# Optimization experiments

Hardware: AMD Instinct MI355X
Metric: run time of the kernel (lower is better)

Reference implementation:

```python
import jax, jax.numpy as jnp
import numpy as np

B, T, D = 2, 2048, 2048
HQ, HKV, HD = 16, 8, 128
GROUP = HQ // HKV
EPS = 1e-6


def rms_norm(x, scale):
    # qwen3-compatible: compute in fp32
    xf = x.astype(jnp.float32)
    var = jnp.mean(xf * xf, axis=-1, keepdims=True)
    return (xf * jax.lax.rsqrt(var + EPS) * scale).astype(x.dtype)


def apply_rope(x, cos, sin):
    # x: [B,H,T,d]; cos,sin: [T,d]
    d2 = x.shape[-1] // 2
    x1, x2 = x[..., :d2], x[..., d2:]
    rot = jnp.concatenate([-x2, x1], axis=-1)
    return (x * cos[None, None] + rot * sin[None, None]).astype(x.dtype)


def setup_inputs() -> dict:
    key = jax.random.key(0)
    ks = jax.random.split(key, 8)
    x = jax.random.normal(ks[0], (B, T, D), dtype=jnp.float32)
    # causal mask: True where attention is disallowed (j > i)
    mask = jnp.triu(jnp.ones((T, T), dtype=jnp.bool_), k=1)
    # RoPE tables
    inv_freq = 1.0 / (10000.0 ** (np.arange(0, HD, 2, dtype=np.float32) / HD))
    pos = np.arange(T, dtype=np.float32)
    ang = np.outer(pos, inv_freq)  # [T, HD/2]
    ang = np.concatenate([ang, ang], axis=-1)  # [T, HD]
    cos = jnp.asarray(np.cos(ang), dtype=jnp.float32)
    sin = jnp.asarray(np.sin(ang), dtype=jnp.float32)
    s = 0.02
    Wq = jax.random.normal(ks[1], (HQ * HD, D), dtype=jnp.float32) * s
    Wk = jax.random.normal(ks[2], (HKV * HD, D), dtype=jnp.float32) * s
    Wv = jax.random.normal(ks[3], (HKV * HD, D), dtype=jnp.float32) * s
    Wo = jax.random.normal(ks[4], (D, HQ * HD), dtype=jnp.float32) * s
    q_scale = jnp.ones((HD,), dtype=jnp.float32)
    k_scale = jnp.ones((HD,), dtype=jnp.float32)
    return {"x": x, "mask": mask, "cos": cos, "sin": sin,
            "Wq": Wq, "Wk": Wk, "Wv": Wv, "Wo": Wo,
            "q_scale": q_scale, "k_scale": k_scale}


def reference(x, mask, cos, sin, Wq, Wk, Wv, Wo, q_scale, k_scale):
    Bc, Tc, _ = x.shape
    Q = jnp.einsum('btd,ed->bte', x, Wq).reshape(Bc, Tc, HQ, HD).transpose(0, 2, 1, 3)
    K = jnp.einsum('btd,ed->bte', x, Wk).reshape(Bc, Tc, HKV, HD).transpose(0, 2, 1, 3)
    V = jnp.einsum('btd,ed->bte', x, Wv).reshape(Bc, Tc, HKV, HD).transpose(0, 2, 1, 3)
    Q = rms_norm(Q, q_scale)
    K = rms_norm(K, k_scale)
    Q = apply_rope(Q, cos, sin)
    K = apply_rope(K, cos, sin)
    K = jnp.repeat(K, GROUP, axis=1)  # [B,HQ,T,d]
    V = jnp.repeat(V, GROUP, axis=1)
    S = jnp.einsum('bhqd,bhkd->bhqk', Q, K) / jnp.sqrt(jnp.float32(HD))
    S = jnp.where(mask[None, None], -jnp.inf, S)
    P = jax.nn.softmax(S, axis=-1)
    ctx = jnp.einsum('bhqk,bhkd->bhqd', P, V).transpose(0, 2, 1, 3).reshape(Bc, Tc, HQ * HD)
    return jnp.einsum('bte,de->btd', ctx, Wo)
```

## Files before the change

kernel.cpp:

```cpp
#include <hip/hip_runtime.h>
#include <cstdint>
#include <cstddef>

#define B_ 2
#define T_ 2048
#define D_ 2048
#define HQ_ 16
#define HKV_ 8
#define HD_ 128

typedef __attribute__((ext_vector_type(8))) short short8;
typedef __attribute__((ext_vector_type(8))) unsigned short ushort8;
typedef __attribute__((ext_vector_type(4))) float f32x4;
typedef __attribute__((ext_vector_type(2))) unsigned short ushort2v;
typedef __attribute__((ext_vector_type(4))) unsigned short ushort4v;
typedef __attribute__((ext_vector_type(2))) float float2v;
typedef __attribute__((ext_vector_type(4))) float float4v;

__device__ __forceinline__ unsigned short f2bf(float f) {
  unsigned int u = __builtin_bit_cast(unsigned int, f);
  u += 0x7fffu + ((u >> 16) & 1u);
  return (unsigned short)(u >> 16);
}
__device__ __forceinline__ float bf2f(unsigned short h) {
  unsigned int u = ((unsigned int)h) << 16;
  return __builtin_bit_cast(float, u);
}

#if defined(__has_builtin)
#if __has_builtin(__builtin_amdgcn_global_load_lds)
#define HAS_GLL 1
#endif
#endif
#ifndef HAS_GLL
#define HAS_GLL 0
#endif

__device__ __forceinline__ void gll16(const void* g, void* l) {
#if HAS_GLL
  __builtin_amdgcn_global_load_lds((const __attribute__((address_space(1))) void*)g,
                                   (__attribute__((address_space(3))) void*)l, 16, 0, 0);
#else
  *(ushort8*)((char*)l + (threadIdx.x & 63) * 16) = *(const ushort8*)g;
#endif
}

__global__ __launch_bounds__(256) void cast_all(const float* __restrict__ x,
                                                const float* __restrict__ wq,
                                                const float* __restrict__ wk,
                                                const float* __restrict__ wv,
                                                const float* __restrict__ wo,
                                                unsigned short* __restrict__ xb,
                                                unsigned short* __restrict__ wqkv,
                                                unsigned short* __restrict__ wob) {
  int i = (blockIdx.x * 256 + threadIdx.x) * 4;
  if (i >= 20971520) return;
  const float* s;
  unsigned short* d;
  int soff, doff;
  if (i < 8388608)       { s = x;  soff = i;            d = xb;   doff = i; }
  else if (i < 12582912) { s = wq; soff = i - 8388608;  d = wqkv; doff = i - 8388608; }
  else if (i < 14680064) { s = wk; soff = i - 12582912; d = wqkv; doff = i - 8388608; }
  else if (i < 16777216) { s = wv; soff = i - 14680064; d = wqkv; doff = i - 8388608; }
  else                   { s = wo; soff = i - 16777216; d = wob;  doff = i - 16777216; }
  float4v v = *(const float4v*)(s + soff);
  ushort4v o; o.x = f2bf(v.x); o.y = f2bf(v.y); o.z = f2bf(v.z); o.w = f2bf(v.w);
  *(ushort4v*)(d + doff) = o;
}

template<int M, int N, int K, bool BF16_OUT>
__global__ __launch_bounds__(256) void gemm_bt(const unsigned short* __restrict__ A,
                                               const unsigned short* __restrict__ W,
                                               void* __restrict__ Cout) {
  __shared__ __align__(16) unsigned short As[128 * 32];
  __shared__ __align__(16) unsigned short Bs[128 * 32];
  const int tid = threadIdx.x;
  const int lane = tid & 63;
  const int wv = tid >> 6;
  const int g = lane >> 4;
  const int c = lane & 15;
  const int m0 = blockIdx.y * 128;
  const int n0 = blockIdx.x * 128;
  const int wm = (wv >> 1) * 64;
  const int wn = (wv & 1) * 64;

  f32x4 acc[4][4];
  for (int i = 0; i < 4; i++)
    for (int j = 0; j < 4; j++) acc[i][j] = (f32x4)0.0f;

  const int ch0 = wv * 64 + lane;
  const int r0 = ch0 >> 2, cc0 = (ch0 & 3) * 8;
  const int ch1 = 256 + ch0;
  const int r1 = ch1 >> 2, cc1 = (ch1 & 3) * 8;
  unsigned short* ldsA0 = As + (size_t)(wv * 64) * 8;
  unsigned short* ldsA1 = As + (size_t)(256 + wv * 64) * 8;
  unsigned short* ldsB0 = Bs + (size_t)(wv * 64) * 8;
  unsigned short* ldsB1 = Bs + (size_t)(256 + wv * 64) * 8;

  for (int k0 = 0; k0 < K; k0 += 32) {
    __syncthreads();
    gll16(&A[(size_t)(m0 + r0) * K + k0 + cc0], ldsA0);
    gll16(&A[(size_t)(m0 + r1) * K + k0 + cc1], ldsA1);
    gll16(&W[(size_t)(n0 + r0) * K + k0 + cc0], ldsB0);
    gll16(&W[(size_t)(n0 + r1) * K + k0 + cc1], ldsB1);
    __syncthreads();
    short8 a[4], b[4];
    for (int i = 0; i < 4; i++) a[i] = *(const short8*)&As[(wm + i * 16 + c) * 32 + g * 8];
    for (int j = 0; j < 4; j++) b[j] = *(const short8*)&Bs[(wn + j * 16 + c) * 32 + g * 8];
    for (int i = 0; i < 4; i++)
      for (int j = 0; j < 4; j++)
        acc[i][j] = __builtin_amdgcn_mfma_f32_16x16x32_bf16(a[i], b[j], acc[i][j], 0, 0, 0);
  }

  for (int i = 0; i < 4; i++)
    for (int j = 0; j < 4; j++)
      for (int r = 0; r < 4; r++) {
        int row = m0 + wm + i * 16 + g * 4 + r;
        int col = n0 + wn + j * 16 + c;
        if (BF16_OUT)
          ((unsigned short*)Cout)[(size_t)row * N + col] = f2bf(acc[i][j][r]);
        else
          ((float*)Cout)[(size_t)row * N + col] = acc[i][j][r];
      }
}

__global__ __launch_bounds__(256) void qk_norm_rope(const unsigned short* __restrict__ qkv,
                                                    const float* __restrict__ cosT,
                                                    const float* __restrict__ sinT,
                                                    const float* __restrict__ q_scale,
                                                    const float* __restrict__ k_scale,
                                                    unsigned short* __restrict__ Qb,
                                                    unsigned short* __restrict__ Kb) {
  const int tid = threadIdx.x;
  const int lane = tid & 63;
  const int wv = tid >> 6;
  const int row = blockIdx.x;
  const int b = row >> 11;
  const int t = row & 2047;
  const int d0 = lane * 2;

  const float2v cs = *(const float2v*)&cosT[t * 128 + d0];
  const float2v sn = *(const float2v*)&sinT[t * 128 + d0];
  const float2v qsc = *(const float2v*)&q_scale[d0];
  const float2v ksc = *(const float2v*)&k_scale[d0];
  const float sgn = (lane < 32) ? -1.0f : 1.0f;
  const unsigned short* base = qkv + (size_t)row * 4096;

#pragma unroll
  for (int s6 = 0; s6 < 6; s6++) {
    const int slot = wv * 6 + s6;
    const bool isQ = slot < 16;
    const unsigned short* src = base + (isQ ? slot * 128 : 2048 + (slot - 16) * 128);
    ushort2v u = *(const ushort2v*)&src[d0];
    float x0 = bf2f(u.x), x1 = bf2f(u.y);
    float ss = x0 * x0 + x1 * x1;
    ss += __shfl_xor(ss, 1);  ss += __shfl_xor(ss, 2);  ss += __shfl_xor(ss, 4);
    ss += __shfl_xor(ss, 8);  ss += __shfl_xor(ss, 16); ss += __shfl_xor(ss, 32);
    float rinv = rsqrtf(ss * (1.0f / 128.0f) + 1e-6f);
    float2v scv = isQ ? qsc : ksc;
    float xn0 = x0 * rinv * scv.x;
    float xn1 = x1 * rinv * scv.y;
    float o0 = __shfl_xor(xn0, 32);
    float o1 = __shfl_xor(xn1, 32);
    float r0v = xn0 * cs.x + sgn * o0 * sn.x;
    float r1v = xn1 * cs.y + sgn * o1 * sn.y;
    ushort2v out; out.x = f2bf(r0v); out.y = f2bf(r1v);
    unsigned short* dst;
    if (isQ) dst = Qb + ((size_t)(b * HQ_ + slot) * T_ + t) * HD_;
    else     dst = Kb + ((size_t)(b * HKV_ + (slot - 16)) * T_ + t) * HD_;
    *(ushort2v*)&dst[d0] = out;
  }
}

__global__ __launch_bounds__(256) void v_transpose(const unsigned short* __restrict__ qkv,
                                                   unsigned short* __restrict__ Vt) {
  __shared__ unsigned short lds[128 * 65];
  const int tid = threadIdx.x;
  const int blk = blockIdx.x;
  const int tblk = blk & 31;
  const int kv = (blk >> 5) & 7;
  const int b = blk >> 8;
  const int t0 = tblk * 64;
  const int r = tid >> 2;
  const int seg = tid & 3;
  const unsigned short* src = qkv + (size_t)(b * T_ + t0 + r) * 4096 + 3072 + kv * 128;
  for (int i = 0; i < 4; i++) {
    int cc = seg * 32 + i * 8;
    ushort8 v = *(const ushort8*)&src[cc];
    for (int q = 0; q < 8; q++) lds[(cc + q) * 65 + r] = v[q];
  }
  __syncthreads();
  const int cI = tid >> 1;
  const int rs = (tid & 1) * 32;
  unsigned short* dst = Vt + ((size_t)(b * HKV_ + kv) * HD_ + cI) * T_ + t0 + rs;
  const unsigned short* srow = &lds[cI * 65 + rs];
  for (int j = 0; j < 32; j += 4) {
    ushort4v v; v.x = srow[j]; v.y = srow[j + 1]; v.z = srow[j + 2]; v.w = srow[j + 3];
    *(ushort4v*)&dst[j] = v;
  }
}

__global__ __launch_bounds__(256) void attn(const unsigned short* __restrict__ Qb,
                                            const unsigned short* __restrict__ Kb,
                                            const unsigned short* __restrict__ Vt,
                                            unsigned short* __restrict__ ctxb) {
  __shared__ __align__(16) unsigned short Ks[64 * 128];
  __shared__ __align__(16) unsigned short Vs[128 * 64];
  __shared__ __align__(16) unsigned short Ps[4][16 * 72];
  const int tid = threadIdx.x;
  const int lane = tid & 63;
  const int wv = tid >> 6;
  const int g = lane >> 4;
  const int c = lane & 15;

  const int blk = blockIdx.x;
  const int kv = blk & 7;
  const int idx = blk >> 3;
  const int p = idx >> 2;
  const int b = (idx >> 1) & 1;
  const int h = kv * 2 + (idx & 1);

  const unsigned short* Kh = Kb + (size_t)(b * HKV_ + kv) * T_ * HD_;
  const unsigned short* Vh = Vt + (size_t)(b * HKV_ + kv) * HD_ * T_;
  const float scale = 0.08838834764831845f;

  for (int ph = 0; ph < 2; ph++) {
    const int qb = ph ? (31 - p) : p;
    const int nkt = qb + 1;
    const unsigned short* Qh = Qb + ((size_t)(b * HQ_ + h) * T_ + qb * 64 + wv * 16) * HD_;

    short8 aq[4];
#pragma unroll
    for (int dk = 0; dk < 4; dk++) aq[dk] = *(const short8*)&Qh[c * HD_ + dk * 32 + g * 8];

    f32x4 acc[8];
#pragma unroll
    for (int dc = 0; dc < 8; dc++) acc[dc] = (f32x4)0.0f;
    float lp[4] = {0.0f, 0.0f, 0.0f, 0.0f};

    for (int kt = 0; kt < nkt; kt++) {
      __syncthreads();
#pragma unroll
      for (int i = 0; i < 4; i++) {
        const int ch = wv * 256 + i * 64 + lane;
        const int rowK = ch >> 4, ccK = ch & 15;
        const int sK = ccK ^ (rowK & 7);
        gll16(Kh + (size_t)(kt * 64 + rowK) * HD_ + sK * 8,
              Ks + (size_t)(wv * 256 + i * 64) * 8);
        const int rowV = ch >> 3, ccV = ch & 7;
        const int sV = ccV ^ (rowV & 7);
        gll16(Vh + (size_t)rowV * T_ + kt * 64 + sV * 8,
              Vs + (size_t)(wv * 256 + i * 64) * 8);
      }
      __syncthreads();

      f32x4 s[4];
#pragma unroll
      for (int kf = 0; kf < 4; kf++) s[kf] = (f32x4)0.0f;
#pragma unroll
      for (int dk = 0; dk < 4; dk++) {
#pragma unroll
        for (int kf = 0; kf < 4; kf++) {
          short8 bk = *(const short8*)&Ks[(kf * 16 + c) * 128 + ((dk * 4 + g) ^ (c & 7)) * 8];
          s[kf] = __builtin_amdgcn_mfma_f32_16x16x32_bf16(aq[dk], bk, s[kf], 0, 0, 0);
        }
      }

      const bool diag = (kt == nkt - 1);
#pragma unroll
      for (int kf = 0; kf < 4; kf++) {
#pragma unroll
        for (int r = 0; r < 4; r++) {
          float pv = __expf(s[kf][r] * scale);
          if (diag) {
            int key = kt * 64 + kf * 16 + c;
            int rowq = qb * 64 + wv * 16 + g * 4 + r;
            if (key > rowq) pv = 0.0f;
          }
          lp[r] += pv;
          Ps[wv][(g * 4 + r) * 72 + kf * 16 + c] = f2bf(pv);
        }
      }

      short8 ap[2];
      ap[0] = *(const short8*)&Ps[wv][c * 72 + g * 8];
      ap[1] = *(const short8*)&Ps[wv][c * 72 + 32 + g * 8];
#pragma unroll
      for (int dc = 0; dc < 8; dc++) {
#pragma unroll
        for (int kf2 = 0; kf2 < 2; kf2++) {
          short8 bv = *(const short8*)&Vs[(dc * 16 + c) * 64 + ((kf2 * 4 + g) ^ (c & 7)) * 8];
          acc[dc] = __builtin_amdgcn_mfma_f32_16x16x32_bf16(ap[kf2], bv, acc[dc], 0, 0, 0);
        }
      }
    }

#pragma unroll
    for (int r = 0; r < 4; r++) {
      float l = lp[r];
      l += __shfl_xor(l, 1); l += __shfl_xor(l, 2);
      l += __shfl_xor(l, 4); l += __shfl_xor(l, 8);
      float inv = 1.0f / l;
      int row = b * T_ + qb * 64 + wv * 16 + g * 4 + r;
#pragma unroll
      for (int dc = 0; dc < 8; dc++)
        ctxb[(size_t)row * (HQ_ * HD_) + h * HD_ + dc * 16 + c] = f2bf(acc[dc][r] * inv);
    }
  }
}

extern "C" void kernel_launch(void* const* d_in, const int* in_sizes, int n_in,
                              void* d_out, int out_size, void* d_ws, size_t ws_size,
                              hipStream_t stream) {
  const float* x = (const float*)d_in[0];
  const float* cosT = (const float*)d_in[2];
  const float* sinT = (const float*)d_in[3];
  const float* Wq = (const float*)d_in[4];
  const float* Wk = (const float*)d_in[5];
  const float* Wv = (const float*)d_in[6];
  const float* Wo = (const float*)d_in[7];
  const float* q_scale = (const float*)d_in[8];
  const float* k_scale = (const float*)d_in[9];

  char* ws = (char*)d_ws;
  unsigned short* qkv  = (unsigned short*)(ws + 0);
  unsigned short* ctxb = qkv;
  unsigned short* xb   = (unsigned short*)(ws + 33554432);
  unsigned short* wqkv = (unsigned short*)(ws + 50331648);
  unsigned short* wob  = (unsigned short*)(ws + 67108864);
  unsigned short* Qb   = (unsigned short*)(ws + 75497472);
  unsigned short* Kb   = (unsigned short*)(ws + 92274688);
  unsigned short* Vt   = (unsigned short*)(ws + 100663296);

  cast_all<<<20480, 256, 0, stream>>>(x, Wq, Wk, Wv, Wo, xb, wqkv, wob);
  gemm_bt<4096, 4096, 2048, true><<<dim3(32, 32), 256, 0, stream>>>(xb, wqkv, qkv);
  qk_norm_rope<<<4096, 256, 0, stream>>>(qkv, cosT, sinT, q_scale, k_scale, Qb, Kb);
  v_transpose<<<512, 256, 0, stream>>>(qkv, Vt);
  attn<<<512, 256, 0, stream>>>(Qb, Kb, Vt, ctxb);
  gemm_bt<4096, 2048, 2048, false><<<dim3(16, 32), 256, 0, stream>>>(ctxb, wob, d_out);
}
```

Baseline: 378.4 us.

## Replace GEMM with 256x256 tile, double-buffered 8-wave pipelined MFMA kernel

The simple 128x128 GEMM, which had single-buffered LDS and a full sync every K step, is replaced by a 512-thread kernel. It computes 256x256 tiles with K=64 double buffering, XOR-swizzled LDS to avoid bank conflicts, and interleaves global-to-LDS loads between MFMA phases under s_setprio and barriers. Workgroup IDs are swizzled into chunks for L2 locality. This raises data reuse per load and hides memory latency, in exchange for heavy register and LDS use (128KB of LDS per block) and fewer workgroups, especially for the N=2048 output GEMM, which launches only 128 blocks.

```diff
diff --git a/kernel.cpp b/kernel.cpp
--- a/kernel.cpp
+++ b/kernel.cpp
@@ -68,60 +68,132 @@
   *(ushort4v*)(d + doff) = o;
 }
 
+#define PH_SYNC { __builtin_amdgcn_s_barrier(); \
+                  asm volatile("s_waitcnt lgkmcnt(0)" ::: "memory"); \
+                  __builtin_amdgcn_sched_barrier(0); \
+                  __builtin_amdgcn_s_setprio(1); }
+#define PH_END  { __builtin_amdgcn_s_setprio(0); \
+                  __builtin_amdgcn_s_barrier(); \
+                  __builtin_amdgcn_sched_barrier(0); }
+
+#define LDA(BUF, QM) { \
+  _Pragma("unroll") for (int ii = 0; ii < 4; ii++) { \
+    _Pragma("unroll") for (int ks = 0; ks < 2; ks++) \
+      a[ii][ks] = *(const short8*)&Abuf[BUF][((QM)*128 + wm*64 + ii*16 + c)*64 + (((ks*4+g)^cs)*8)]; } }
+
+#define LDB(BUF, QN, BB) { \
+  _Pragma("unroll") for (int jj = 0; jj < 2; jj++) { \
+    _Pragma("unroll") for (int ks = 0; ks < 2; ks++) \
+      BB[jj][ks] = *(const short8*)&Bbuf[BUF][((QN)*128 + wn*32 + jj*16 + c)*64 + (((ks*4+g)^cs)*8)]; } }
+
+#define MM(QM, QN, BB) { \
+  _Pragma("unroll") for (int ii = 0; ii < 4; ii++) { \
+    _Pragma("unroll") for (int jj = 0; jj < 2; jj++) { \
+      f32x4 t_ = __builtin_amdgcn_mfma_f32_16x16x32_bf16(a[ii][0], BB[jj][0], acc[(QM)*4+ii][(QN)*2+jj], 0, 0, 0); \
+      acc[(QM)*4+ii][(QN)*2+jj] = __builtin_amdgcn_mfma_f32_16x16x32_bf16(a[ii][1], BB[jj][1], t_, 0, 0, 0); } } }
+
 template<int M, int N, int K, bool BF16_OUT>
-__global__ __launch_bounds__(256) void gemm_bt(const unsigned short* __restrict__ A,
-                                               const unsigned short* __restrict__ W,
-                                               void* __restrict__ Cout) {
-  __shared__ __align__(16) unsigned short As[128 * 32];
-  __shared__ __align__(16) unsigned short Bs[128 * 32];
+__global__ __launch_bounds__(512, 2) void gemm8(const unsigned short* __restrict__ A,
+                                                const unsigned short* __restrict__ W,
+                                                void* __restrict__ Cout) {
+  __shared__ __align__(16) unsigned short Abuf[2][256 * 64];
+  __shared__ __align__(16) unsigned short Bbuf[2][256 * 64];
   const int tid = threadIdx.x;
   const int lane = tid & 63;
   const int wv = tid >> 6;
   const int g = lane >> 4;
   const int c = lane & 15;
-  const int m0 = blockIdx.y * 128;
-  const int n0 = blockIdx.x * 128;
-  const int wm = (wv >> 1) * 64;
-  const int wn = (wv & 1) * 64;
-
-  f32x4 acc[4][4];
-  for (int i = 0; i < 4; i++)
+  const int cs = c & 7;
+  const int wm = wv >> 2;
+  const int wn = wv & 3;
+
+  constexpr int NT = N / 256;
+  constexpr int NWG = (M / 256) * NT;
+  constexpr int CHUNK = NWG / 8;
+  const int bid = blockIdx.x;
+  const int swz = (bid & 7) * CHUNK + (bid >> 3);
+  const int m0 = (swz / NT) * 256;
+  const int n0 = (swz % NT) * 256;
+
+  const int prl = wv * 8 + (lane >> 3);
+  const int scl = lane & 7;
+#define STA(BUF, P0, KO) { \
+    int pr_ = (P0) + prl; \
+    int lr_ = ((pr_ >> 6) & 1) * 128 + ((pr_ >> 7) & 1) * 64 + (pr_ & 63); \
+    int lc_ = (scl ^ (pr_ & 7)) * 8; \
+    gll16(&A[(size_t)(m0 + lr_) * K + (KO) + lc_], &Abuf[BUF][(P0) * 64 + wv * 512]); }
+#define STB(BUF, P0, KO) { \
+    int pr_ = (P0) + prl; \
+    int lr_ = ((pr_ >> 5) & 3) * 64 + ((pr_ >> 7) & 1) * 32 + (pr_ & 31); \
+    int lc_ = (scl ^ (pr_ & 7)) * 8; \
+    gll16(&W[(size_t)(n0 + lr_) * K + (KO) + lc_], &Bbuf[BUF][(P0) * 64 + wv * 512]); }
+
+  short8 a[4][2], b0[2][2], b1[2][2];
+  f32x4 acc[8][4];
+#pragma unroll
+  for (int i = 0; i < 8; i++)
+#pragma unroll
     for (int j = 0; j < 4; j++) acc[i][j] = (f32x4)0.0f;
 
-  const int ch0 = wv * 64 + lane;
-  const int r0 = ch0 >> 2, cc0 = (ch0 & 3) * 8;
-  const int ch1 = 256 + ch0;
-  const int r1 = ch1 >> 2, cc1 = (ch1 & 3) * 8;
-  unsigned short* ldsA0 = As + (size_t)(wv * 64) * 8;
-  unsigned short* ldsA1 = As + (size_t)(256 + wv * 64) * 8;
-  unsigned short* ldsB0 = Bs + (size_t)(wv * 64) * 8;
-  unsigned short* ldsB1 = Bs + (size_t)(256 + wv * 64) * 8;
-
-  for (int k0 = 0; k0 < K; k0 += 32) {
-    __syncthreads();
-    gll16(&A[(size_t)(m0 + r0) * K + k0 + cc0], ldsA0);
-    gll16(&A[(size_t)(m0 + r1) * K + k0 + cc1], ldsA1);
-    gll16(&W[(size_t)(n0 + r0) * K + k0 + cc0], ldsB0);
-    gll16(&W[(size_t)(n0 + r1) * K + k0 + cc1], ldsB1);
-    __syncthreads();
-    short8 a[4], b[4];
-    for (int i = 0; i < 4; i++) a[i] = *(const short8*)&As[(wm + i * 16 + c) * 32 + g * 8];
-    for (int j = 0; j < 4; j++) b[j] = *(const short8*)&Bs[(wn + j * 16 + c) * 32 + g * 8];
-    for (int i = 0; i < 4; i++)
-      for (int j = 0; j < 4; j++)
-        acc[i][j] = __builtin_amdgcn_mfma_f32_16x16x32_bf16(a[i], b[j], acc[i][j], 0, 0, 0);
+  STA(0, 0, 0); STA(0, 64, 0); STA(0, 128, 0); STA(0, 192, 0);
+  STB(0, 0, 0); STB(0, 64, 0); STB(0, 128, 0); STB(0, 192, 0);
+  STA(1, 0, 64); STA(1, 64, 64); STA(1, 128, 64); STA(1, 192, 64);
+  STB(1, 0, 64); STB(1, 64, 64); STB(1, 128, 64); STB(1, 192, 64);
+  asm volatile("s_waitcnt vmcnt(8)" ::: "memory");
+  __builtin_amdgcn_s_barrier();
+
+  constexpr int NITER = K / 128;
+  for (int it = 0; it < NITER - 1; ++it) {
+    const int k2 = it * 128 + 128;
+    const int k3 = k2 + 64;
+    LDA(0, 0); LDB(0, 0, b0);
+    PH_SYNC; MM(0, 0, b0); PH_END;
+    LDB(0, 1, b1);
+    STA(0, 0, k2); STA(0, 64, k2); STB(0, 0, k2); STB(0, 64, k2);
+    PH_SYNC; MM(0, 1, b1); PH_END;
+    LDA(0, 1);
+    STB(0, 128, k2); STB(0, 192, k2);
+    PH_SYNC; MM(1, 1, b1); PH_END;
+    STA(0, 128, k2); STA(0, 192, k2);
+    asm volatile("s_waitcnt vmcnt(8)" ::: "memory");
+    PH_SYNC; MM(1, 0, b0); PH_END;
+    LDA(1, 0); LDB(1, 0, b0);
+    PH_SYNC; MM(0, 0, b0); PH_END;
+    LDB(1, 1, b1);
+    STA(1, 0, k3); STA(1, 64, k3); STB(1, 0, k3); STB(1, 64, k3);
+    PH_SYNC; MM(0, 1, b1); PH_END;
+    LDA(1, 1);
+    STB(1, 128, k3); STB(1, 192, k3);
+    PH_SYNC; MM(1, 1, b1); PH_END;
+    STA(1, 128, k3); STA(1, 192, k3);
+    asm volatile("s_waitcnt vmcnt(8)" ::: "memory");
+    PH_SYNC; MM(1, 0, b0); PH_END;
   }
-
-  for (int i = 0; i < 4; i++)
-    for (int j = 0; j < 4; j++)
+  LDA(0, 0); LDB(0, 0, b0); PH_SYNC; MM(0, 0, b0); PH_END;
+  LDB(0, 1, b1);            PH_SYNC; MM(0, 1, b1); PH_END;
+  LDA(0, 1);                PH_SYNC; MM(1, 1, b1); PH_END;
+  asm volatile("s_waitcnt vmcnt(0)" ::: "memory");
+  PH_SYNC; MM(1, 0, b0); PH_END;
+  LDA(1, 0); LDB(1, 0, b0); PH_SYNC; MM(0, 0, b0); PH_END;
+  LDB(1, 1, b1);            PH_SYNC; MM(0, 1, b1); PH_END;
+  LDA(1, 1);                PH_SYNC; MM(1, 1, b1); PH_END;
+  PH_SYNC; MM(1, 0, b0); PH_END;
+
+#pragma unroll
+  for (int I = 0; I < 8; I++)
+#pragma unroll
+    for (int J = 0; J < 4; J++)
+#pragma unroll
       for (int r = 0; r < 4; r++) {
-        int row = m0 + wm + i * 16 + g * 4 + r;
-        int col = n0 + wn + j * 16 + c;
+        int row = m0 + wm * 128 + I * 16 + g * 4 + r;
+        int col = n0 + wn * 64 + J * 16 + c;
         if (BF16_OUT)
-          ((unsigned short*)Cout)[(size_t)row * N + col] = f2bf(acc[i][j][r]);
+          ((unsigned short*)Cout)[(size_t)row * N + col] = f2bf(acc[I][J][r]);
         else
-          ((float*)Cout)[(size_t)row * N + col] = acc[i][j][r];
+          ((float*)Cout)[(size_t)row * N + col] = acc[I][J][r];
       }
+#undef STA
+#undef STB
 }
 
 __global__ __launch_bounds__(256) void qk_norm_rope(const unsigned short* __restrict__ qkv,
@@ -333,9 +405,9 @@
   unsigned short* Vt   = (unsigned short*)(ws + 100663296);
 
   cast_all<<<20480, 256, 0, stream>>>(x, Wq, Wk, Wv, Wo, xb, wqkv, wob);
-  gemm_bt<4096, 4096, 2048, true><<<dim3(32, 32), 256, 0, stream>>>(xb, wqkv, qkv);
+  gemm8<4096, 4096, 2048, true><<<256, 512, 0, stream>>>(xb, wqkv, qkv);
   qk_norm_rope<<<4096, 256, 0, stream>>>(qkv, cosT, sinT, q_scale, k_scale, Qb, Kb);
   v_transpose<<<512, 256, 0, stream>>>(qkv, Vt);
   attn<<<512, 256, 0, stream>>>(Qb, Kb, Vt, ctxb);
-  gemm_bt<4096, 2048, 2048, false><<<dim3(16, 32), 256, 0, stream>>>(ctxb, wob, d_out);
-}
+  gemm8<4096, 2048, 2048, false><<<128, 512, 0, stream>>>(ctxb, wob, d_out);
+}
```

After: 357.2 us. 5.6% less time.
